# Optimization experiments

Hardware: AMD Instinct MI355X
Metric: run time of the kernel (lower is better)

Reference implementation:

```python
import jax, jax.numpy as jnp
import numpy as np
from jax import lax

VOCAB = 32000
D = 256      # d_model
N = 16       # n_neurons
NL = 6       # n_layers
DS = 16      # d_state
DC = 4       # d_conv
DI = 512     # d_inner = expand * d_model
DTR = 16     # dt_rank = ceil(D/16)
NH = 4       # attention heads
HD = D // NH
B, L = 1, 128


def setup_inputs() -> dict:
    key = jax.random.key(0)
    ks = list(jax.random.split(key, 32))
    it = iter(ks)

    def rn(shape, scale):
        return jax.random.normal(next(it), shape, jnp.float32) * scale

    p = {}
    p["x"] = jax.random.randint(next(it), (B, L), 0, VOCAB, dtype=jnp.int32)
    p["embedding"] = rn((VOCAB, D), 0.02)
    p["norm1_w"] = jnp.ones((NL, D)); p["norm1_b"] = jnp.zeros((NL, D))
    p["norm2_w"] = jnp.ones((NL, D)); p["norm2_b"] = jnp.zeros((NL, D))
    # Mamba params (stacked over layers)
    p["in_proj_w"] = rn((NL, 2 * DI, D), D ** -0.5)
    p["conv_w"] = rn((NL, DI, DC), DC ** -0.5)
    p["conv_b"] = jnp.zeros((NL, DI))
    p["x_proj_w"] = rn((NL, DTR + 2 * DS, DI), DI ** -0.5)
    p["dt_proj_w"] = rn((NL, DI, DTR), DTR ** -0.5)
    dt0 = jax.random.uniform(next(it), (NL, DI), jnp.float32, 1e-3, 1e-1)
    p["dt_proj_b"] = jnp.log(jnp.expm1(dt0))  # inverse softplus init
    p["A_log"] = jnp.log(jnp.tile(jnp.arange(1.0, DS + 1.0, dtype=jnp.float32), (NL, DI, 1)))
    p["skip_D"] = jnp.ones((NL, DI))
    p["out_proj_w"] = rn((NL, D, DI), DI ** -0.5)
    # cross-neuron MHA params
    p["attn_in_w"] = rn((NL, 3 * D, D), D ** -0.5)
    p["attn_in_b"] = jnp.zeros((NL, 3 * D))
    p["attn_out_w"] = rn((NL, D, D), D ** -0.5)
    p["attn_out_b"] = jnp.zeros((NL, D))
    p["norm_f_w"] = jnp.ones((D,)); p["norm_f_b"] = jnp.zeros((D,))
    p["head_b"] = jnp.zeros((VOCAB,))
    return p


def _ln(x, w, b):
    m = x.mean(-1, keepdims=True)
    v = ((x - m) ** 2).mean(-1, keepdims=True)
    return (x - m) * lax.rsqrt(v + 1e-5) * w + b


def _mamba(x, ipw, cw, cb, xpw, dpw, dpb, alog, dskip, opw):
    # x: (BN, L, D)
    BN, Ls, _ = x.shape
    xz = x @ ipw.T                       # (BN, L, 2*DI)
    u, z = xz[..., :DI], xz[..., DI:]
    # depthwise causal conv1d, kernel DC, left-pad DC-1
    uc = lax.conv_general_dilated(
        u.swapaxes(1, 2), cw[:, None, :], (1,), [(DC - 1, 0)],
        dimension_numbers=("NCH", "OIH", "NCH"), feature_group_count=DI)
    u = jax.nn.silu(uc + cb[None, :, None]).swapaxes(1, 2)  # (BN, L, DI)
    xdbl = u @ xpw.T                     # (BN, L, DTR+2*DS)
    dt = jax.nn.softplus(xdbl[..., :DTR] @ dpw.T + dpb)     # (BN, L, DI)
    Bm = xdbl[..., DTR:DTR + DS]
    Cm = xdbl[..., DTR + DS:]
    A = -jnp.exp(alog)                   # (DI, DS)

    def step(h, ins):
        dt_t, b_t, c_t, u_t = ins        # (BN,DI) (BN,DS) (BN,DS) (BN,DI)
        h = jnp.exp(dt_t[..., None] * A) * h + (dt_t * u_t)[..., None] * b_t[:, None, :]
        return h, jnp.einsum("bds,bs->bd", h, c_t)

    h0 = jnp.zeros((BN, DI, DS), x.dtype)
    _, ys = lax.scan(step, h0, (dt.swapaxes(0, 1), Bm.swapaxes(0, 1),
                                Cm.swapaxes(0, 1), u.swapaxes(0, 1)))
    y = ys.swapaxes(0, 1) + u * dskip
    return (y * jax.nn.silu(z)) @ opw.T


def _mha(x, iw, ib, ow, ob):
    # x: (B*L, N, D); self-attention across neurons
    Bq, S, _ = x.shape
    qkv = x @ iw.T + ib
    q, k, v = jnp.split(qkv, 3, axis=-1)
    q = q.reshape(Bq, S, NH, HD); k = k.reshape(Bq, S, NH, HD); v = v.reshape(Bq, S, NH, HD)
    att = jax.nn.softmax(jnp.einsum("bqhd,bkhd->bhqk", q, k) / np.float32(np.sqrt(HD)), axis=-1)
    o = jnp.einsum("bhqk,bkhd->bqhd", att, v).reshape(Bq, S, D)
    return o @ ow.T + ob


def reference(x, embedding, norm1_w, norm1_b, norm2_w, norm2_b, in_proj_w, conv_w,
              conv_b, x_proj_w, dt_proj_w, dt_proj_b, A_log, skip_D, out_proj_w,
              attn_in_w, attn_in_b, attn_out_w, attn_out_b, norm_f_w, norm_f_b, head_b):
    Bb, Ll = x.shape
    h = embedding[x]                                             # (B, L, D)
    h = jnp.broadcast_to(h[:, None], (Bb, N, Ll, D)).reshape(Bb * N, Ll, D)
    for i in range(NL):
        h = h + _mamba(_ln(h, norm1_w[i], norm1_b[i]), in_proj_w[i], conv_w[i],
                       conv_b[i], x_proj_w[i], dt_proj_w[i], dt_proj_b[i],
                       A_log[i], skip_D[i], out_proj_w[i])
        xc = _ln(h, norm2_w[i], norm2_b[i]).reshape(Bb, N, Ll, D)
        xc = xc.transpose(0, 2, 1, 3).reshape(Bb * Ll, N, D)
        co = _mha(xc, attn_in_w[i], attn_in_b[i], attn_out_w[i], attn_out_b[i])
        h = h + co.reshape(Bb, Ll, N, D).transpose(0, 2, 1, 3).reshape(Bb * N, Ll, D)
    h = h.reshape(Bb, N, Ll, D).mean(axis=1)                     # avg over neurons
    return _ln(h, norm_f_w, norm_f_b) @ embedding.T + head_b     # tied head
```

## Files before the change

kernel.cpp:

```cpp
#include <hip/hip_runtime.h>

constexpr int SEQ    = 128;
constexpr int NVOCAB = 32000;

constexpr size_t O_HA = 0;
constexpr size_t O_HB = O_HA + (size_t)SEQ*256;
constexpr size_t O_U  = O_HB + (size_t)SEQ*256;
constexpr size_t O_DT = O_U  + (size_t)SEQ*512;
constexpr size_t O_ZS = O_DT + (size_t)SEQ*512;
constexpr size_t O_BC = O_ZS + (size_t)SEQ*512;
constexpr size_t O_YG = O_BC + (size_t)SEQ*32;
constexpr size_t O_AH = O_YG + (size_t)SEQ*512;

__device__ __forceinline__ float wsum(float p) {
    #pragma unroll
    for (int m = 1; m < 64; m <<= 1) p += __shfl_xor(p, m);
    return p;
}
__device__ __forceinline__ float dot4(float4 a, float4 b) {
    return a.x*b.x + a.y*b.y + a.z*b.z + a.w*b.w;
}

template<int MR, int KK>
__device__ __forceinline__ void gemmX(
    const float* __restrict__ Wg, const float* __restrict__ A, int AS,
    float* __restrict__ dest, int DS,
    const float* __restrict__ addsrc, int ASS, const float* __restrict__ bias)
{
    const int lane = threadIdx.x & 63;
    const int wv   = threadIdx.x >> 6;
    const int tq = lane & 3, cs = lane >> 2;
    const int c  = wv*16 + cs;
    const float* Wp = Wg + (size_t)c*KK + tq*8;
    float acc[MR];
    #pragma unroll
    for (int r = 0; r < MR; ++r) acc[r] = 0.0f;

    float4 w0a = *(const float4*)(Wp);
    float4 w0b = *(const float4*)(Wp + 4);
    float4 w1a, w1b;
    #pragma unroll
    for (int kc = 0; kc < KK; kc += 64) {
        if (kc + 32 < KK) {
            w1a = *(const float4*)(Wp + kc + 32);
            w1b = *(const float4*)(Wp + kc + 36);
        }
        #pragma unroll
        for (int r = 0; r < MR; ++r) {
            float4 a0 = *(const float4*)&A[r*AS + kc + tq*8];
            float4 a1 = *(const float4*)&A[r*AS + kc + tq*8 + 4];
            acc[r] += dot4(a0, w0a) + dot4(a1, w0b);
        }
        if (kc + 64 < KK) {
            w0a = *(const float4*)(Wp + kc + 64);
            w0b = *(const float4*)(Wp + kc + 68);
        }
        if (kc + 32 < KK) {
            #pragma unroll
            for (int r = 0; r < MR; ++r) {
                float4 a0 = *(const float4*)&A[r*AS + kc + 32 + tq*8];
                float4 a1 = *(const float4*)&A[r*AS + kc + 36 + tq*8];
                acc[r] += dot4(a0, w1a) + dot4(a1, w1b);
            }
        }
    }
    #pragma unroll
    for (int r = 0; r < MR; ++r) {
        float v = acc[r];
        v += __shfl_xor(v, 1);
        v += __shfl_xor(v, 2);
        acc[r] = v;
    }
    if (tq == 0) {
        #pragma unroll
        for (int r = 0; r < MR; ++r) {
            float v = acc[r];
            if (bias)   v += bias[c];
            if (addsrc) v += addsrc[r*ASS + c];
            dest[r*DS + c] = v;
        }
    }
}

__device__ __forceinline__ void ln_row(const float* __restrict__ src, float* __restrict__ dst,
                                       const float* __restrict__ w, const float* __restrict__ b)
{
    int lane = threadIdx.x & 63;
    float4 x = *(const float4*)&src[lane*4];
    float sm = wsum(x.x + x.y + x.z + x.w);
    float mean = sm * (1.0f/256.0f);
    float d0 = x.x-mean, d1 = x.y-mean, d2 = x.z-mean, d3 = x.w-mean;
    float var = wsum(d0*d0 + d1*d1 + d2*d2 + d3*d3) * (1.0f/256.0f);
    float rstd = rsqrtf(var + 1e-5f);
    float4 ww = *(const float4*)&w[lane*4];
    float4 bb = *(const float4*)&b[lane*4];
    float4 o;
    o.x = d0*rstd*ww.x + bb.x;
    o.y = d1*rstd*ww.y + bb.y;
    o.z = d2*rstd*ww.z + bb.z;
    o.w = d3*rstd*ww.w + bb.w;
    *(float4*)&dst[lane*4] = o;
}

__global__ __launch_bounds__(1024) void rowk_kernel(
    const int* __restrict__ x, const float* __restrict__ emb,
    const float* __restrict__ n1w_l, const float* __restrict__ n1b_l,
    const float* __restrict__ n2w_l, const float* __restrict__ n2b_l,
    const float* __restrict__ ipw_l, const float* __restrict__ cw_l, const float* __restrict__ cb_l,
    const float* __restrict__ xpw_l, const float* __restrict__ dpw_l, const float* __restrict__ dpb_l,
    const float* __restrict__ opw_l, const float* __restrict__ aivw_l, const float* __restrict__ aivb_l,
    const float* __restrict__ aow_l, const float* __restrict__ aob_l,
    const float* __restrict__ nfw, const float* __restrict__ nfb,
    const float* __restrict__ hin, float* __restrict__ hout,
    const float* __restrict__ ygv, float* __restrict__ uv, float* __restrict__ dtv,
    float* __restrict__ zsv, float* __restrict__ bcv, float* __restrict__ AH,
    int li)
{
    __shared__ float SM[6336];
    float* hP  = SM;
    float* h1  = SM + 1056;
    float* sLN = SM + 2112;
    float* sAX = SM + 3168;
    float* zR  = SM + 5248;
    float* suR = SM + 5760;
    float* sxR = SM + 6272;

    const int r = blockIdx.x;
    const int tid = threadIdx.x;
    const int lane = tid & 63, wv = tid >> 6;
    int rr[4];
    #pragma unroll
    for (int j = 0; j < 4; ++j) { int v = r - 3 + j; rr[j] = v < 0 ? 0 : v; }

    {
        int hr = tid >> 8, hc = tid & 255;
        if (li <= 1) hP[hr*264 + hc] = emb[(size_t)x[rr[hr]]*256 + hc];
        else         hP[hr*264 + hc] = hin[rr[hr]*256 + hc];
    }
    __syncthreads();

    float* hC = hP;
    if (li >= 1) {
        {
            int yr = tid >> 9, yc = tid & 511;
            sAX[yr*520 + yc]     = ygv[rr[yr]*512 + yc];
            sAX[(2+yr)*520 + yc] = ygv[rr[2+yr]*512 + yc];
        }
        __syncthreads();
        gemmX<4,512>(opw_l, sAX, 520, h1, 264, hP, 264, nullptr);
        __syncthreads();
        if (wv < 4) ln_row(h1 + wv*264, sLN + wv*264, n2w_l, n2b_l);
        __syncthreads();
        gemmX<4,256>(aivw_l, sLN, 264, sAX, 520, nullptr, 0, aivb_l);
        __syncthreads();
        gemmX<4,256>(aow_l, sAX, 520, h1, 264, h1, 264, aob_l);
        __syncthreads();
        hC = h1;
        if (tid < 256) hout[r*256 + tid] = h1[3*264 + tid];
        if (li == 6) {
            if (tid < 256) {
                float v = h1[3*264 + tid];
                float s = wsum(v);
                float q = wsum(v*v);
                if (lane == 0) { sxR[wv] = s; sxR[8 + wv] = q; }
            }
            __syncthreads();
            if (tid < 256) {
                float v = h1[3*264 + tid];
                float mean = (sxR[0]+sxR[1]+sxR[2]+sxR[3]) * (1.0f/256.0f);
                float var  = (sxR[8]+sxR[9]+sxR[10]+sxR[11]) * (1.0f/256.0f) - mean*mean;
                float rstd = rsqrtf(var + 1e-5f);
                AH[r*256 + tid] = (v - mean)*rstd*nfw[tid] + nfb[tid];
            }
            return;
        }
    }

    if (wv < 4) ln_row(hC + wv*264, sLN + wv*264, n1w_l, n1b_l);
    __syncthreads();
    gemmX<4,256>(ipw_l,                   sLN, 264, sAX,       520, nullptr, 0, nullptr);
    __syncthreads();
    gemmX<4,256>(ipw_l + (size_t)256*256, sLN, 264, sAX + 256, 520, nullptr, 0, nullptr);
    __syncthreads();
    gemmX<1,256>(ipw_l + (size_t)512*256, sLN + 3*264, 264, zR,       512, nullptr, 0, nullptr);
    __syncthreads();
    gemmX<1,256>(ipw_l + (size_t)768*256, sLN + 3*264, 264, zR + 256, 512, nullptr, 0, nullptr);
    __syncthreads();

    if (tid < 512) {
        int d = tid;
        float4 c4 = *(const float4*)&cw_l[d*4];
        float acc = cb_l[d];
        if (r >= 3) acc += sAX[d]        * c4.x;
        if (r >= 2) acc += sAX[520 + d]  * c4.y;
        if (r >= 1) acc += sAX[1040 + d] * c4.z;
        acc += sAX[1560 + d] * c4.w;
        float sg = acc / (1.0f + __expf(-acc));
        suR[d] = sg;
        uv[r*512 + d] = sg;
        float z = zR[d];
        zsv[r*512 + d] = z / (1.0f + __expf(-z));
    }
    __syncthreads();

    {
        float4 a0 = *(const float4*)&suR[lane*4];
        float4 a1 = *(const float4*)&suR[256 + lane*4];
        float p[3];
        #pragma unroll
        for (int j = 0; j < 3; ++j) {
            int c = wv*3 + j;
            float4 q0 = *(const float4*)&xpw_l[(size_t)c*512 + lane*4];
            float4 q1 = *(const float4*)&xpw_l[(size_t)c*512 + 256 + lane*4];
            p[j] = dot4(a0, q0) + dot4(a1, q1);
        }
        #pragma unroll
        for (int m = 1; m < 64; m <<= 1) {
            #pragma unroll
            for (int j = 0; j < 3; ++j) p[j] += __shfl_xor(p[j], m);
        }
        if (lane == 0) {
            #pragma unroll
            for (int j = 0; j < 3; ++j) sxR[wv*3 + j] = p[j];
        }
    }
    __syncthreads();
    if (tid >= 16 && tid < 48) bcv[r*32 + tid - 16] = sxR[tid];

    if (tid < 512) {
        int d = tid;
        float4 sx0 = *(const float4*)&sxR[0];
        float4 sx1 = *(const float4*)&sxR[4];
        float4 sx2 = *(const float4*)&sxR[8];
        float4 sx3 = *(const float4*)&sxR[12];
        const float4* dp = (const float4*)&dpw_l[(size_t)d*16];
        float acc = dpb_l[d] + dot4(dp[0], sx0) + dot4(dp[1], sx1)
                             + dot4(dp[2], sx2) + dot4(dp[3], sx3);
        dtv[r*512 + d] = fmaxf(acc, 0.0f) + log1pf(__expf(-fabsf(acc)));
    }
}

__global__ __launch_bounds__(256) void scan_kernel(
    const float* __restrict__ dt, const float* __restrict__ u, const float* __restrict__ zs,
    const float* __restrict__ bcv,
    const float* __restrict__ alog_l, const float* __restrict__ dsk_l,
    float* __restrict__ yg)
{
    __shared__ float s5[5*128];
    float* sdt = s5;        float* su2 = s5 + 128;
    float* sz2 = s5 + 256;  float* sB  = s5 + 384;  float* sC = s5 + 512;
    int tid = threadIdx.x;
    int s  = tid & 15, dl = tid >> 4;
    int d0 = blockIdx.x * 16;
    int d  = d0 + dl;
    float a_ds = -__expf(alog_l[d*16 + s]);
    float dskv = dsk_l[d];
    float hst = 0.0f;
    for (int t0 = 0; t0 < SEQ; t0 += 8) {
        __syncthreads();
        if (tid < 128) {
            int tt = tid >> 4, j = tid & 15;
            int t = t0 + tt;
            sdt[tt*16+j] = dt[t*512 + d0 + j];
            su2[tt*16+j] = u [t*512 + d0 + j];
            sz2[tt*16+j] = zs[t*512 + d0 + j];
        } else {
            int q = tid - 128;
            int tt = q >> 4, j = q & 15;
            int t = t0 + tt;
            sB[tt*16+j] = bcv[t*32 + j];
            sC[tt*16+j] = bcv[t*32 + 16 + j];
        }
        __syncthreads();
        #pragma unroll
        for (int tt = 0; tt < 8; ++tt) {
            float dtvv = sdt[tt*16+dl];
            float uvv  = su2[tt*16+dl];
            hst = __expf(dtvv * a_ds) * hst + dtvv * uvv * sB[tt*16+s];
            float p = hst * sC[tt*16+s];
            p += __shfl_xor(p, 1);
            p += __shfl_xor(p, 2);
            p += __shfl_xor(p, 4);
            p += __shfl_xor(p, 8);
            if (s == 0) {
                float y = p + uvv * dskv;
                yg[(t0+tt)*512 + d] = y * sz2[tt*16+dl];
            }
        }
    }
}

__global__ __launch_bounds__(256) void head_kernel(
    const float* __restrict__ AH, const float* __restrict__ emb,
    const float* __restrict__ hb, float* __restrict__ out)
{
    __shared__ float sA[32*129];
    __shared__ float sW[32*129];
    int tid = threadIdx.x;
    int c0 = blockIdx.x * 128;
    int rr = tid >> 1;
    int kj = (tid & 1) * 16;
    int r4 = (tid >> 4) * 4;
    int c4 = (tid & 15) * 4;
    float acc[8][8] = {};

    for (int kc = 0; kc < 256; kc += 32) {
        __syncthreads();
        #pragma unroll
        for (int i = 0; i < 4; ++i) {
            float4 a = *(const float4*)&AH[(size_t)rr*256 + kc + kj + i*4];
            sA[(kj+i*4+0)*129 + rr] = a.x;
            sA[(kj+i*4+1)*129 + rr] = a.y;
            sA[(kj+i*4+2)*129 + rr] = a.z;
            sA[(kj+i*4+3)*129 + rr] = a.w;
            float4 w = *(const float4*)&emb[(size_t)(c0+rr)*256 + kc + kj + i*4];
            sW[(kj+i*4+0)*129 + rr] = w.x;
            sW[(kj+i*4+1)*129 + rr] = w.y;
            sW[(kj+i*4+2)*129 + rr] = w.z;
            sW[(kj+i*4+3)*129 + rr] = w.w;
        }
        __syncthreads();
        #pragma unroll
        for (int k = 0; k < 32; ++k) {
            float4 a0 = *(const float4*)&sA[k*129 + r4];
            float4 a1 = *(const float4*)&sA[k*129 + 64 + r4];
            float4 b0 = *(const float4*)&sW[k*129 + c4];
            float4 b1 = *(const float4*)&sW[k*129 + 64 + c4];
            float av[8] = {a0.x,a0.y,a0.z,a0.w, a1.x,a1.y,a1.z,a1.w};
            float bv[8] = {b0.x,b0.y,b0.z,b0.w, b1.x,b1.y,b1.z,b1.w};
            #pragma unroll
            for (int i = 0; i < 8; ++i)
                #pragma unroll
                for (int j = 0; j < 8; ++j)
                    acc[i][j] += av[i]*bv[j];
        }
    }
    #pragma unroll
    for (int i = 0; i < 8; ++i) {
        int r = (i < 4) ? (r4 + i) : (64 + r4 + i - 4);
        #pragma unroll
        for (int jh = 0; jh < 2; ++jh) {
            int c = c0 + jh*64 + c4;
            float4 h4 = *(const float4*)&hb[c];
            float4 o;
            o.x = acc[i][jh*4+0] + h4.x;
            o.y = acc[i][jh*4+1] + h4.y;
            o.z = acc[i][jh*4+2] + h4.z;
            o.w = acc[i][jh*4+3] + h4.w;
            *(float4*)&out[(size_t)r*NVOCAB + c] = o;
        }
    }
}

extern "C" void kernel_launch(void* const* d_in, const int* in_sizes, int n_in,
                              void* d_out, int out_size, void* d_ws, size_t ws_size,
                              hipStream_t stream)
{
    const int*   xin = (const int*)d_in[0];
    const float* emb = (const float*)d_in[1];
    const float* n1w = (const float*)d_in[2];
    const float* n1b = (const float*)d_in[3];
    const float* n2w = (const float*)d_in[4];
    const float* n2b = (const float*)d_in[5];
    const float* ipw = (const float*)d_in[6];
    const float* cw  = (const float*)d_in[7];
    const float* cb  = (const float*)d_in[8];
    const float* xpw = (const float*)d_in[9];
    const float* dpw = (const float*)d_in[10];
    const float* dpb = (const float*)d_in[11];
    const float* alog= (const float*)d_in[12];
    const float* dsk = (const float*)d_in[13];
    const float* opw = (const float*)d_in[14];
    const float* aiw = (const float*)d_in[15];
    const float* aib = (const float*)d_in[16];
    const float* aow = (const float*)d_in[17];
    const float* aob = (const float*)d_in[18];
    const float* nfw = (const float*)d_in[19];
    const float* nfb = (const float*)d_in[20];
    const float* hb  = (const float*)d_in[21];
    float* ws  = (float*)d_ws;
    float* out = (float*)d_out;

    for (int i = 0; i <= 6; ++i) {
        int ka = i <= 5 ? i : 5;
        int kc = i >= 1 ? i - 1 : 0;
        const float* hin  = (i % 2 == 0) ? ws + O_HA : ws + O_HB;
        float*       hout = (i % 2 == 0) ? ws + O_HB : ws + O_HA;
        rowk_kernel<<<128, 1024, 0, stream>>>(
            xin, emb,
            n1w + ka*256, n1b + ka*256,
            n2w + kc*256, n2b + kc*256,
            ipw + (size_t)ka*1024*256, cw + (size_t)ka*512*4, cb + ka*512,
            xpw + (size_t)ka*48*512, dpw + (size_t)ka*512*16, dpb + ka*512,
            opw + (size_t)kc*256*512,
            aiw + (size_t)kc*768*256 + (size_t)512*256, aib + kc*768 + 512,
            aow + (size_t)kc*256*256, aob + kc*256,
            nfw, nfb,
            hin, hout,
            ws + O_YG, ws + O_U, ws + O_DT, ws + O_ZS, ws + O_BC, ws + O_AH,
            i);
        if (i <= 5)
            scan_kernel<<<32, 256, 0, stream>>>(
                ws + O_DT, ws + O_U, ws + O_ZS, ws + O_BC,
                alog + (size_t)i*512*16, dsk + i*512, ws + O_YG);
    }
    head_kernel<<<NVOCAB/128, 256, 0, stream>>>(ws + O_AH, emb, hb, out);
}
```

Before: 582.1 us.

## Use bf16 MFMA for tied head and split-K the per-row GEMMs

The fp32 tiled vocab-head GEMM is replaced by a bf16 MFMA 16x16x32 kernel. A new conversion kernel casts the embedding table to bf16 on every call, and the final layernorm output is written as bf16. The in-block row GEMMs are reorganised into a 4-way split-K: each wave computes 4 columns, and partial sums are reduced through shared memory with an extra barrier. This adds a 32000x256 conversion pass each call and lowers head precision to bf16.

```diff
diff --git a/kernel.cpp b/kernel.cpp
--- a/kernel.cpp
+++ b/kernel.cpp
@@ -1,4 +1,8 @@
 #include <hip/hip_runtime.h>
+#include <hip/hip_bf16.h>
+
+typedef __bf16 bf16x8 __attribute__((ext_vector_type(8)));
+typedef float f32x4 __attribute__((ext_vector_type(4)));
 
 constexpr int SEQ    = 128;
 constexpr int NVOCAB = 32000;
@@ -11,6 +15,7 @@
 constexpr size_t O_BC = O_ZS + (size_t)SEQ*512;
 constexpr size_t O_YG = O_BC + (size_t)SEQ*32;
 constexpr size_t O_AH = O_YG + (size_t)SEQ*512;
+constexpr size_t O_EB = O_AH + (size_t)SEQ*256;
 
 __device__ __forceinline__ float wsum(float p) {
     #pragma unroll
@@ -22,59 +27,90 @@
 }
 
 template<int MR, int KK>
-__device__ __forceinline__ void gemmX(
+__device__ __forceinline__ void gemmS(
     const float* __restrict__ Wg, const float* __restrict__ A, int AS,
-    float* __restrict__ dest, int DS,
+    float* __restrict__ pb, float* __restrict__ dest, int DS,
     const float* __restrict__ addsrc, int ASS, const float* __restrict__ bias)
 {
-    const int lane = threadIdx.x & 63;
-    const int wv   = threadIdx.x >> 6;
+    const int tid  = threadIdx.x;
+    const int lane = tid & 63;
+    const int wv   = tid >> 6;
+    const int kg   = wv >> 2;
+    const int cg   = wv & 3;
     const int tq = lane & 3, cs = lane >> 2;
-    const int c  = wv*16 + cs;
-    const float* Wp = Wg + (size_t)c*KK + tq*8;
-    float acc[MR];
-    #pragma unroll
-    for (int r = 0; r < MR; ++r) acc[r] = 0.0f;
-
-    float4 w0a = *(const float4*)(Wp);
-    float4 w0b = *(const float4*)(Wp + 4);
-    float4 w1a, w1b;
-    #pragma unroll
-    for (int kc = 0; kc < KK; kc += 64) {
-        if (kc + 32 < KK) {
-            w1a = *(const float4*)(Wp + kc + 32);
-            w1b = *(const float4*)(Wp + kc + 36);
-        }
+    const int c0 = cg*64 + cs*4;
+    constexpr int KQ  = KK/4;
+    constexpr int NCH = KQ/16;
+    const int kb = kg*KQ;
+    const float* W0 = Wg + (size_t)(c0+0)*KK + kb + tq*4;
+    const float* W1 = Wg + (size_t)(c0+1)*KK + kb + tq*4;
+    const float* W2 = Wg + (size_t)(c0+2)*KK + kb + tq*4;
+    const float* W3 = Wg + (size_t)(c0+3)*KK + kb + tq*4;
+
+    float acc[MR][4];
+    #pragma unroll
+    for (int r = 0; r < MR; ++r)
+        #pragma unroll
+        for (int j = 0; j < 4; ++j) acc[r][j] = 0.0f;
+
+    float4 e0 = *(const float4*)(W0);
+    float4 e1 = *(const float4*)(W1);
+    float4 e2 = *(const float4*)(W2);
+    float4 e3 = *(const float4*)(W3);
+    float4 o0, o1, o2, o3;
+
+    #pragma unroll
+    for (int ch = 0; ch < NCH; ch += 2) {
+        o0 = *(const float4*)(W0 + (ch+1)*16);
+        o1 = *(const float4*)(W1 + (ch+1)*16);
+        o2 = *(const float4*)(W2 + (ch+1)*16);
+        o3 = *(const float4*)(W3 + (ch+1)*16);
         #pragma unroll
         for (int r = 0; r < MR; ++r) {
-            float4 a0 = *(const float4*)&A[r*AS + kc + tq*8];
-            float4 a1 = *(const float4*)&A[r*AS + kc + tq*8 + 4];
-            acc[r] += dot4(a0, w0a) + dot4(a1, w0b);
-        }
-        if (kc + 64 < KK) {
-            w0a = *(const float4*)(Wp + kc + 64);
-            w0b = *(const float4*)(Wp + kc + 68);
-        }
-        if (kc + 32 < KK) {
+            float4 a = *(const float4*)&A[r*AS + kb + ch*16 + tq*4];
+            acc[r][0] += dot4(a, e0);
+            acc[r][1] += dot4(a, e1);
+            acc[r][2] += dot4(a, e2);
+            acc[r][3] += dot4(a, e3);
+        }
+        if (ch + 2 < NCH) {
+            e0 = *(const float4*)(W0 + (ch+2)*16);
+            e1 = *(const float4*)(W1 + (ch+2)*16);
+            e2 = *(const float4*)(W2 + (ch+2)*16);
+            e3 = *(const float4*)(W3 + (ch+2)*16);
+        }
+        #pragma unroll
+        for (int r = 0; r < MR; ++r) {
+            float4 a = *(const float4*)&A[r*AS + kb + (ch+1)*16 + tq*4];
+            acc[r][0] += dot4(a, o0);
+            acc[r][1] += dot4(a, o1);
+            acc[r][2] += dot4(a, o2);
+            acc[r][3] += dot4(a, o3);
+        }
+    }
+    #pragma unroll
+    for (int r = 0; r < MR; ++r)
+        #pragma unroll
+        for (int j = 0; j < 4; ++j) {
+            float v = acc[r][j];
+            v += __shfl_xor(v, 1);
+            v += __shfl_xor(v, 2);
+            acc[r][j] = v;
+        }
+    if (tq == 0) {
+        #pragma unroll
+        for (int r = 0; r < MR; ++r)
             #pragma unroll
-            for (int r = 0; r < MR; ++r) {
-                float4 a0 = *(const float4*)&A[r*AS + kc + 32 + tq*8];
-                float4 a1 = *(const float4*)&A[r*AS + kc + 36 + tq*8];
-                acc[r] += dot4(a0, w1a) + dot4(a1, w1b);
-            }
-        }
-    }
-    #pragma unroll
-    for (int r = 0; r < MR; ++r) {
-        float v = acc[r];
-        v += __shfl_xor(v, 1);
-        v += __shfl_xor(v, 2);
-        acc[r] = v;
-    }
-    if (tq == 0) {
+            for (int j = 0; j < 4; ++j)
+                pb[(kg*MR + r)*256 + c0 + j] = acc[r][j];
+    }
+    __syncthreads();
+    if (tid < 256) {
+        int c = tid;
         #pragma unroll
         for (int r = 0; r < MR; ++r) {
-            float v = acc[r];
+            float v = pb[(0*MR + r)*256 + c] + pb[(1*MR + r)*256 + c]
+                    + pb[(2*MR + r)*256 + c] + pb[(3*MR + r)*256 + c];
             if (bias)   v += bias[c];
             if (addsrc) v += addsrc[r*ASS + c];
             dest[r*DS + c] = v;
@@ -102,6 +138,20 @@
     *(float4*)&dst[lane*4] = o;
 }
 
+__global__ __launch_bounds__(256) void cvt_emb_kernel(const float* __restrict__ e,
+                                                      __hip_bfloat16* __restrict__ o)
+{
+    size_t base = (size_t)(blockIdx.x * 256 + threadIdx.x) * 16;
+    #pragma unroll
+    for (int j = 0; j < 16; j += 4) {
+        float4 v = *(const float4*)&e[base + j];
+        o[base + j + 0] = __float2bfloat16(v.x);
+        o[base + j + 1] = __float2bfloat16(v.y);
+        o[base + j + 2] = __float2bfloat16(v.z);
+        o[base + j + 3] = __float2bfloat16(v.w);
+    }
+}
+
 __global__ __launch_bounds__(1024) void rowk_kernel(
     const int* __restrict__ x, const float* __restrict__ emb,
     const float* __restrict__ n1w_l, const float* __restrict__ n1b_l,
@@ -113,10 +163,10 @@
     const float* __restrict__ nfw, const float* __restrict__ nfb,
     const float* __restrict__ hin, float* __restrict__ hout,
     const float* __restrict__ ygv, float* __restrict__ uv, float* __restrict__ dtv,
-    float* __restrict__ zsv, float* __restrict__ bcv, float* __restrict__ AH,
+    float* __restrict__ zsv, float* __restrict__ bcv, __hip_bfloat16* __restrict__ AHb,
     int li)
 {
-    __shared__ float SM[6336];
+    __shared__ float SM[10432];
     float* hP  = SM;
     float* h1  = SM + 1056;
     float* sLN = SM + 2112;
@@ -124,6 +174,7 @@
     float* zR  = SM + 5248;
     float* suR = SM + 5760;
     float* sxR = SM + 6272;
+    float* pb  = SM + 6336;
 
     const int r = blockIdx.x;
     const int tid = threadIdx.x;
@@ -147,13 +198,13 @@
             sAX[(2+yr)*520 + yc] = ygv[rr[2+yr]*512 + yc];
         }
         __syncthreads();
-        gemmX<4,512>(opw_l, sAX, 520, h1, 264, hP, 264, nullptr);
+        gemmS<4,512>(opw_l, sAX, 520, pb, h1, 264, hP, 264, nullptr);
         __syncthreads();
         if (wv < 4) ln_row(h1 + wv*264, sLN + wv*264, n2w_l, n2b_l);
         __syncthreads();
-        gemmX<4,256>(aivw_l, sLN, 264, sAX, 520, nullptr, 0, aivb_l);
-        __syncthreads();
-        gemmX<4,256>(aow_l, sAX, 520, h1, 264, h1, 264, aob_l);
+        gemmS<4,256>(aivw_l, sLN, 264, pb, sAX, 520, nullptr, 0, aivb_l);
+        __syncthreads();
+        gemmS<4,256>(aow_l, sAX, 520, pb, h1, 264, h1, 264, aob_l);
         __syncthreads();
         hC = h1;
         if (tid < 256) hout[r*256 + tid] = h1[3*264 + tid];
@@ -170,7 +221,7 @@
                 float mean = (sxR[0]+sxR[1]+sxR[2]+sxR[3]) * (1.0f/256.0f);
                 float var  = (sxR[8]+sxR[9]+sxR[10]+sxR[11]) * (1.0f/256.0f) - mean*mean;
                 float rstd = rsqrtf(var + 1e-5f);
-                AH[r*256 + tid] = (v - mean)*rstd*nfw[tid] + nfb[tid];
+                AHb[r*256 + tid] = __float2bfloat16((v - mean)*rstd*nfw[tid] + nfb[tid]);
             }
             return;
         }
@@ -178,13 +229,13 @@
 
     if (wv < 4) ln_row(hC + wv*264, sLN + wv*264, n1w_l, n1b_l);
     __syncthreads();
-    gemmX<4,256>(ipw_l,                   sLN, 264, sAX,       520, nullptr, 0, nullptr);
-    __syncthreads();
-    gemmX<4,256>(ipw_l + (size_t)256*256, sLN, 264, sAX + 256, 520, nullptr, 0, nullptr);
-    __syncthreads();
-    gemmX<1,256>(ipw_l + (size_t)512*256, sLN + 3*264, 264, zR,       512, nullptr, 0, nullptr);
-    __syncthreads();
-    gemmX<1,256>(ipw_l + (size_t)768*256, sLN + 3*264, 264, zR + 256, 512, nullptr, 0, nullptr);
+    gemmS<4,256>(ipw_l,                   sLN, 264, pb, sAX,       520, nullptr, 0, nullptr);
+    __syncthreads();
+    gemmS<4,256>(ipw_l + (size_t)256*256, sLN, 264, pb, sAX + 256, 520, nullptr, 0, nullptr);
+    __syncthreads();
+    gemmS<1,256>(ipw_l + (size_t)512*256, sLN + 3*264, 264, pb, zR,       512, nullptr, 0, nullptr);
+    __syncthreads();
+    gemmS<1,256>(ipw_l + (size_t)768*256, sLN + 3*264, 264, pb, zR + 256, 512, nullptr, 0, nullptr);
     __syncthreads();
 
     if (tid < 512) {
@@ -290,66 +341,33 @@
     }
 }
 
-__global__ __launch_bounds__(256) void head_kernel(
-    const float* __restrict__ AH, const float* __restrict__ emb,
+__global__ __launch_bounds__(256) void head_mfma_kernel(
+    const __hip_bfloat16* __restrict__ AHb, const __hip_bfloat16* __restrict__ Eb,
     const float* __restrict__ hb, float* __restrict__ out)
 {
-    __shared__ float sA[32*129];
-    __shared__ float sW[32*129];
     int tid = threadIdx.x;
-    int c0 = blockIdx.x * 128;
-    int rr = tid >> 1;
-    int kj = (tid & 1) * 16;
-    int r4 = (tid >> 4) * 4;
-    int c4 = (tid & 15) * 4;
-    float acc[8][8] = {};
-
-    for (int kc = 0; kc < 256; kc += 32) {
-        __syncthreads();
-        #pragma unroll
-        for (int i = 0; i < 4; ++i) {
-            float4 a = *(const float4*)&AH[(size_t)rr*256 + kc + kj + i*4];
-            sA[(kj+i*4+0)*129 + rr] = a.x;
-            sA[(kj+i*4+1)*129 + rr] = a.y;
-            sA[(kj+i*4+2)*129 + rr] = a.z;
-            sA[(kj+i*4+3)*129 + rr] = a.w;
-            float4 w = *(const float4*)&emb[(size_t)(c0+rr)*256 + kc + kj + i*4];
-            sW[(kj+i*4+0)*129 + rr] = w.x;
-            sW[(kj+i*4+1)*129 + rr] = w.y;
-            sW[(kj+i*4+2)*129 + rr] = w.z;
-            sW[(kj+i*4+3)*129 + rr] = w.w;
-        }
-        __syncthreads();
-        #pragma unroll
-        for (int k = 0; k < 32; ++k) {
-            float4 a0 = *(const float4*)&sA[k*129 + r4];
-            float4 a1 = *(const float4*)&sA[k*129 + 64 + r4];
-            float4 b0 = *(const float4*)&sW[k*129 + c4];
-            float4 b1 = *(const float4*)&sW[k*129 + 64 + c4];
-            float av[8] = {a0.x,a0.y,a0.z,a0.w, a1.x,a1.y,a1.z,a1.w};
-            float bv[8] = {b0.x,b0.y,b0.z,b0.w, b1.x,b1.y,b1.z,b1.w};
-            #pragma unroll
-            for (int i = 0; i < 8; ++i)
-                #pragma unroll
-                for (int j = 0; j < 8; ++j)
-                    acc[i][j] += av[i]*bv[j];
-        }
-    }
-    #pragma unroll
-    for (int i = 0; i < 8; ++i) {
-        int r = (i < 4) ? (r4 + i) : (64 + r4 + i - 4);
-        #pragma unroll
-        for (int jh = 0; jh < 2; ++jh) {
-            int c = c0 + jh*64 + c4;
-            float4 h4 = *(const float4*)&hb[c];
-            float4 o;
-            o.x = acc[i][jh*4+0] + h4.x;
-            o.y = acc[i][jh*4+1] + h4.y;
-            o.z = acc[i][jh*4+2] + h4.z;
-            o.w = acc[i][jh*4+3] + h4.w;
-            *(float4*)&out[(size_t)r*NVOCAB + c] = o;
-        }
-    }
+    int lane = tid & 63;
+    int wv = tid >> 6;
+    int mbase = blockIdx.y * 16;
+    int nbase = blockIdx.x * 64 + wv * 16;
+    int m = mbase + (lane & 15);
+    int n = nbase + (lane & 15);
+    int k0 = (lane >> 4) * 8;
+    const __bf16* Ap = (const __bf16*)AHb + m*256 + k0;
+    const __bf16* Bp = (const __bf16*)Eb + (size_t)n*256 + k0;
+    f32x4 acc = {0.0f, 0.0f, 0.0f, 0.0f};
+    #pragma unroll
+    for (int kb = 0; kb < 256; kb += 32) {
+        bf16x8 a  = *(const bf16x8*)(Ap + kb);
+        bf16x8 bb = *(const bf16x8*)(Bp + kb);
+        acc = __builtin_amdgcn_mfma_f32_16x16x32_bf16(a, bb, acc, 0, 0, 0);
+    }
+    int col = lane & 15;
+    int rq = lane >> 4;
+    float bias = hb[nbase + col];
+    #pragma unroll
+    for (int i = 0; i < 4; ++i)
+        out[(size_t)(mbase + rq*4 + i)*NVOCAB + nbase + col] = acc[i] + bias;
 }
 
 extern "C" void kernel_launch(void* const* d_in, const int* in_sizes, int n_in,
@@ -381,6 +399,11 @@
     float* ws  = (float*)d_ws;
     float* out = (float*)d_out;
 
+    __hip_bfloat16* AHb = (__hip_bfloat16*)(ws + O_AH);
+    __hip_bfloat16* Eb  = (__hip_bfloat16*)(ws + O_EB);
+
+    cvt_emb_kernel<<<2000, 256, 0, stream>>>(emb, Eb);
+
     for (int i = 0; i <= 6; ++i) {
         int ka = i <= 5 ? i : 5;
         int kc = i >= 1 ? i - 1 : 0;
@@ -397,12 +420,12 @@
             aow + (size_t)kc*256*256, aob + kc*256,
             nfw, nfb,
             hin, hout,
-            ws + O_YG, ws + O_U, ws + O_DT, ws + O_ZS, ws + O_BC, ws + O_AH,
+            ws + O_YG, ws + O_U, ws + O_DT, ws + O_ZS, ws + O_BC, AHb,
             i);
         if (i <= 5)
             scan_kernel<<<32, 256, 0, stream>>>(
                 ws + O_DT, ws + O_U, ws + O_ZS, ws + O_BC,
                 alog + (size_t)i*512*16, dsk + i*512, ws + O_YG);
     }
-    head_kernel<<<NVOCAB/128, 256, 0, stream>>>(ws + O_AH, emb, hb, out);
-}
+    head_mfma_kernel<<<dim3(NVOCAB/64, SEQ/16), 256, 0, stream>>>(AHb, Eb, hb, out);
+}
```

After: 774.6 us. +33.1%, slower.
